# Kernel tuning notes

Hardware: AMD Instinct MI355X
Metric: run time of the kernel (lower is better)

## Reference

```python
import jax, jax.numpy as jnp
import numpy as np

B, T, VOCAB = 65536, 34, 14
D_MODEL, TOK_DIM, POS_DIM, QK_DIM, FFN = 5, 2, 3, 5, 2
MAX_DIGITS = 10
EPS = 1e-5


def setup_inputs() -> dict:
    key = jax.random.key(0)
    ks = jax.random.split(key, 8)
    return dict(
        idx=jax.random.randint(ks[0], (B, T), 0, VOCAB),
        tok_A=jnp.float32(2.5), tok_start=jnp.float32(-1.2), tok_stride=jnp.float32(0.29),
        sp_amp=jnp.float32(3.5), sp_phase=jnp.float32(0.0), sp_slope=jnp.float32(0.15), sp_offset=jnp.float32(0.0),
        norm_w=jnp.ones((D_MODEL,), jnp.float32),
        q_w=jax.random.normal(ks[1], (QK_DIM, POS_DIM), jnp.float32) * 0.5,
        q_phase=jnp.zeros((1,), jnp.float32),
        out_A=jax.random.normal(ks[2], (D_MODEL, 1), jnp.float32) * 0.45,
        out_B=jax.random.normal(ks[3], (1, D_MODEL), jnp.float32) * 0.2,
        fc1_w=jax.random.normal(ks[4], (FFN, D_MODEL), jnp.float32) * 0.4,
        fc2_w=jax.random.normal(ks[5], (D_MODEL, FFN), jnp.float32) * 0.4,
        head_w=jax.random.normal(ks[6], (TOK_DIM, D_MODEL), jnp.float32) * 0.4,
    )


def rmsnorm(x, w):
    rms = jnp.sqrt(jnp.mean(x * x, axis=-1, keepdims=True) + EPS)
    return x / rms * w


def micro_forward(idx, tok_A, tok_start, tok_stride, sp_amp, sp_phase, sp_slope, sp_offset,
                  norm_w, q_w, q_phase, out_A, out_B, fc1_w, fc2_w, head_w):
    # token arc embedding table (V, 2)
    d = jnp.arange(VOCAB, dtype=jnp.float32)
    ang = tok_start + d * tok_stride
    tok_emb = jnp.stack([tok_A * jnp.cos(ang), tok_A * jnp.sin(ang)], axis=-1)
    # spiral positional embedding (T, 3)
    t = jnp.arange(T, dtype=jnp.float32)
    th = 2.0 * jnp.pi * t / MAX_DIGITS + sp_phase
    pos = jnp.stack([sp_amp * jnp.cos(th), sp_amp * jnp.sin(th), sp_slope * t + sp_offset], axis=-1)
    # embed: concat token (B,T,2) + position (T,3) -> (B,T,5)
    x = jnp.concatenate([tok_emb[idx], jnp.broadcast_to(pos, (idx.shape[0], T, POS_DIM))], axis=-1)
    # attention (pre-norm); q/k from positions only (qk_input='pos'), shared across batch
    h = rmsnorm(x, norm_w)
    k = pos @ q_w.T                       # (T, QK)
    c, s = jnp.cos(q_phase[0]), jnp.sin(q_phase[0])
    q = k.at[:, 0].set(c * k[:, 0] - s * k[:, 1]).at[:, 1].set(s * k[:, 0] + c * k[:, 1])
    scores = (q @ k.T) / jnp.sqrt(jnp.float32(QK_DIM))   # (T, T)
    causal = jnp.tril(jnp.ones((T, T), bool))
    attn = jax.nn.softmax(jnp.where(causal, scores, -1e9), axis=-1)
    attn_out = jnp.einsum('ts,bsd->btd', attn, h)         # v = normed x (head_dim = d_model)
    x = x + (attn_out @ out_A) @ out_B                    # rank-1 out_proj, residual
    # FFN (pre-norm, 2 hidden units)
    h2 = rmsnorm(x, norm_w)
    x = x + jax.nn.relu(h2 @ fc1_w.T) @ fc2_w.T
    # head: project to token plane, read out against arc embedding table
    hf = rmsnorm(x, norm_w)
    logits = (hf @ head_w.T) @ tok_emb.T                  # (B, T, V)
    return logits


def reference(idx, tok_A, tok_start, tok_stride, sp_amp, sp_phase, sp_slope, sp_offset,
              norm_w, q_w, q_phase, out_A, out_B, fc1_w, fc2_w, head_w):
    return micro_forward(idx, tok_A, tok_start, tok_stride, sp_amp, sp_phase, sp_slope, sp_offset,
                         norm_w, q_w, q_phase, out_A, out_B, fc1_w, fc2_w, head_w)
```

## Files before the change

### kernel.cpp

```cpp
#include <hip/hip_runtime.h>
#include <math.h>

#define T 34
#define V 14
#define NT 256
#define NBLK 1088
#define NWAVES 4352
#define KTILES 8
#define NPAIRS 4
#define LIM (65536 * 34)

typedef float f32x4 __attribute__((ext_vector_type(4)));

__global__ __launch_bounds__(NT, 4) void micro_fused(
    const int* __restrict__ idx, float* __restrict__ out,
    const float* __restrict__ p_tokA, const float* __restrict__ p_tokStart,
    const float* __restrict__ p_tokStride, const float* __restrict__ p_spAmp,
    const float* __restrict__ p_spPhase, const float* __restrict__ p_spSlope,
    const float* __restrict__ p_spOffset, const float* __restrict__ norm_w,
    const float* __restrict__ q_w, const float* __restrict__ q_phase,
    const float* __restrict__ out_A, const float* __restrict__ out_B,
    const float* __restrict__ fc1_w, const float* __restrict__ fc2_w,
    const float* __restrict__ head_w)
{
    __shared__ float G_lds[V * 35];
    __shared__ float TE_lds[V * 2];
    __shared__ float POS_lds[T * 3];
    __shared__ float gbW[4][2][104];
    __shared__ float stageAll[4 * 896];

    const int tid = threadIdx.x;
    const int w = tid >> 6, lane = tid & 63;
    const int wid = blockIdx.x * 4 + w;

    float* sA = stageAll;
    float* sK = stageAll + 1200;
    float* sQ = stageAll + 1370;

    if (tid < V) {
        float ang = p_tokStart[0] + (float)tid * p_tokStride[0];
        TE_lds[2 * tid]     = p_tokA[0] * cosf(ang);
        TE_lds[2 * tid + 1] = p_tokA[0] * sinf(ang);
    }
    if (tid < T) {
        float th = (float)tid * 0.62831853071795864769f + p_spPhase[0];
        float p0 = p_spAmp[0] * cosf(th), p1 = p_spAmp[0] * sinf(th);
        float p2 = p_spSlope[0] * (float)tid + p_spOffset[0];
        POS_lds[3 * tid] = p0; POS_lds[3 * tid + 1] = p1; POS_lds[3 * tid + 2] = p2;
        float kk[5];
        #pragma unroll
        for (int i = 0; i < 5; ++i)
            kk[i] = p0 * q_w[3 * i] + p1 * q_w[3 * i + 1] + p2 * q_w[3 * i + 2];
        float cc = cosf(q_phase[0]), ss = sinf(q_phase[0]);
        #pragma unroll
        for (int i = 0; i < 5; ++i) sK[tid * 5 + i] = kk[i];
        sQ[tid * 5 + 0] = cc * kk[0] - ss * kk[1];
        sQ[tid * 5 + 1] = ss * kk[0] + cc * kk[1];
        sQ[tid * 5 + 2] = kk[2]; sQ[tid * 5 + 3] = kk[3]; sQ[tid * 5 + 4] = kk[4];
    }
    __syncthreads();

    for (int e = tid; e < T * T; e += NT) {
        unsigned tt = (unsigned)e / (unsigned)T;
        unsigned s  = (unsigned)e - tt * T;
        float d = 0.f;
        #pragma unroll
        for (int i = 0; i < 5; ++i) d += sQ[tt * 5 + i] * sK[s * 5 + i];
        sA[tt * 35 + s] = (s <= tt) ? d * 0.44721359549995793928f : 0.f;
    }
    for (int e = tid; e < V * 35; e += NT) {
        int v = e / 35, s = e - v * 35;
        float g = 0.f;
        if (s < T) {
            float x0 = TE_lds[2*v], x1 = TE_lds[2*v+1];
            float x2 = POS_lds[3*s], x3 = POS_lds[3*s+1], x4 = POS_lds[3*s+2];
            float ms = (x0*x0 + x1*x1 + x2*x2 + x3*x3 + x4*x4) * 0.2f;
            float r = rsqrtf(ms + 1e-5f);
            g = (x0 * norm_w[0] * out_A[0] + x1 * norm_w[1] * out_A[1]
               + x2 * norm_w[2] * out_A[2] + x3 * norm_w[3] * out_A[3]
               + x4 * norm_w[4] * out_A[4]) * r;
        }
        G_lds[e] = g;
    }
    __syncthreads();

    const int t = (wid * 64 + lane) % T;
    float A[T];
    #pragma unroll
    for (int s = 0; s < T; ++s) A[s] = sA[t * 35 + s];
    {
        float mx = -1e30f;
        #pragma unroll
        for (int s = 0; s < T; ++s) if (s <= t) mx = fmaxf(mx, A[s]);
        float sum = 0.f;
        #pragma unroll
        for (int s = 0; s < T; ++s) {
            float e2 = (s <= t) ? expf(A[s] - mx) : 0.f;
            A[s] = e2;
            sum += e2;
        }
        float inv = 1.f / sum;
        #pragma unroll
        for (int s = 0; s < T; ++s) A[s] *= inv;
    }
    const float ps0 = POS_lds[3*t], ps1 = POS_lds[3*t+1], ps2 = POS_lds[3*t+2];
    float te0[V], te1[V];
    #pragma unroll
    for (int v = 0; v < V; ++v) { te0[v] = TE_lds[2*v]; te1[v] = TE_lds[2*v+1]; }
    __syncthreads();

    const float nw0 = norm_w[0], nw1 = norm_w[1], nw2 = norm_w[2], nw3 = norm_w[3], nw4 = norm_w[4];
    const float oB0 = out_B[0], oB1 = out_B[1], oB2 = out_B[2], oB3 = out_B[3], oB4 = out_B[4];
    float w1[2][5], hw[2][5], w20[5], w21[5];
    #pragma unroll
    for (int j = 0; j < 2; ++j)
        #pragma unroll
        for (int d = 0; d < 5; ++d) { w1[j][d] = fc1_w[j*5+d]; hw[j][d] = head_w[j*5+d]; }
    #pragma unroll
    for (int d = 0; d < 5; ++d) { w20[d] = fc2_w[2*d]; w21[d] = fc2_w[2*d+1]; }

    const int s_a = (lane < T) ? lane : lane - T;
    const int i2 = lane + 64;
    const int s_b = (i2 < 68) ? i2 - 34 : i2 - 68;
    const bool act2 = (i2 < 102);

    float* gbA = gbW[w][0];
    float* gbB = gbW[w][1];
    float* stg = stageAll + w * 896;
    float2* stg2 = reinterpret_cast<float2*>(stg);
    const f32x4* st4 = reinterpret_cast<const f32x4*>(stg);

    auto computeItem = [&](int tile, int rbase, int curtok, const float* gbT) {
        float acc0 = 0.f, acc1 = 0.f;
        const float2* gbp = reinterpret_cast<const float2*>(gbT + rbase);
        #pragma unroll
        for (int s = 0; s < 17; ++s) {
            float2 gg = gbp[s];
            acc0 = fmaf(A[2*s],   gg.x, acc0);
            acc1 = fmaf(A[2*s+1], gg.y, acc1);
        }
        float acc = acc0 + acc1;

        float2 te = *reinterpret_cast<const float2*>(&TE_lds[curtok * 2]);
        float x0 = te.x + acc * oB0;
        float x1 = te.y + acc * oB1;
        float x2 = ps0 + acc * oB2;
        float x3 = ps1 + acc * oB3;
        float x4 = ps2 + acc * oB4;

        float ms = (x0*x0 + x1*x1 + x2*x2 + x3*x3 + x4*x4) * 0.2f;
        float rr = rsqrtf(ms + 1e-5f);
        float h0 = x0*rr*nw0, h1 = x1*rr*nw1, h2 = x2*rr*nw2, h3 = x3*rr*nw3, h4 = x4*rr*nw4;
        float f0 = fmaxf(0.f, h0*w1[0][0] + h1*w1[0][1] + h2*w1[0][2] + h3*w1[0][3] + h4*w1[0][4]);
        float f1 = fmaxf(0.f, h0*w1[1][0] + h1*w1[1][1] + h2*w1[1][2] + h3*w1[1][3] + h4*w1[1][4]);
        x0 += f0*w20[0] + f1*w21[0];
        x1 += f0*w20[1] + f1*w21[1];
        x2 += f0*w20[2] + f1*w21[2];
        x3 += f0*w20[3] + f1*w21[3];
        x4 += f0*w20[4] + f1*w21[4];

        ms = (x0*x0 + x1*x1 + x2*x2 + x3*x3 + x4*x4) * 0.2f;
        rr = rsqrtf(ms + 1e-5f);
        h0 = x0*rr*nw0; h1 = x1*rr*nw1; h2 = x2*rr*nw2; h3 = x3*rr*nw3; h4 = x4*rr*nw4;
        float p0 = h0*hw[0][0] + h1*hw[0][1] + h2*hw[0][2] + h3*hw[0][3] + h4*hw[0][4];
        float p1 = h0*hw[1][0] + h1*hw[1][1] + h2*hw[1][2] + h3*hw[1][3] + h4*hw[1][4];

        #pragma unroll
        for (int j = 0; j < 7; ++j) {
            float2 o2;
            o2.x = p0 * te0[2*j]   + p1 * te1[2*j];
            o2.y = p0 * te0[2*j+1] + p1 * te1[2*j+1];
            stg2[lane * 7 + j] = o2;
        }
        f32x4* outp = reinterpret_cast<f32x4*>(out) + (size_t)tile * 224;
        __builtin_nontemporal_store(st4[lane],       outp + lane);
        __builtin_nontemporal_store(st4[lane + 64],  outp + lane + 64);
        __builtin_nontemporal_store(st4[lane + 128], outp + lane + 128);
        if (lane < 32)
            __builtin_nontemporal_store(st4[lane + 192], outp + lane + 192);
    };

    int tileA = wid, tileB = wid + NWAVES;
    int b0A = (tileA * 64) / T, b0B = (tileB * 64) / T;
    int tk0A = idx[b0A * T + lane];
    int tk1A = idx[min(b0A * T + lane + 64, LIM - 1)];
    int tkoA = idx[tileA * 64 + lane];
    int tk0B = idx[b0B * T + lane];
    int tk1B = idx[min(b0B * T + lane + 64, LIM - 1)];
    int tkoB = idx[tileB * 64 + lane];

    #pragma unroll
    for (int it = 0; it < NPAIRS; ++it) {
        gbA[lane] = G_lds[tk0A * 35 + s_a];
        if (act2) gbA[i2] = G_lds[tk1A * 35 + s_b];
        gbB[lane] = G_lds[tk0B * 35 + s_a];
        if (act2) gbB[i2] = G_lds[tk1B * 35 + s_b];

        const int rbA = ((tileA * 64 + lane) / T - b0A) * T;
        const int rbB = ((tileB * 64 + lane) / T - b0B) * T;
        const int ctA = tkoA, ctB = tkoB;
        const int tA = tileA, tB = tileB;

        if (it < NPAIRS - 1) {
            tileA += 2 * NWAVES; tileB += 2 * NWAVES;
            b0A = (tileA * 64) / T; b0B = (tileB * 64) / T;
            tk0A = idx[b0A * T + lane];
            tk1A = idx[min(b0A * T + lane + 64, LIM - 1)];
            tkoA = idx[tileA * 64 + lane];
            tk0B = idx[b0B * T + lane];
            tk1B = idx[min(b0B * T + lane + 64, LIM - 1)];
            tkoB = idx[tileB * 64 + lane];
        }

        computeItem(tA, rbA, ctA, gbA);
        computeItem(tB, rbB, ctB, gbB);
    }
}

extern "C" void kernel_launch(void* const* d_in, const int* in_sizes, int n_in,
                              void* d_out, int out_size, void* d_ws, size_t ws_size,
                              hipStream_t stream) {
    const int*   idx        = (const int*)  d_in[0];
    const float* tok_A      = (const float*)d_in[1];
    const float* tok_start  = (const float*)d_in[2];
    const float* tok_stride = (const float*)d_in[3];
    const float* sp_amp     = (const float*)d_in[4];
    const float* sp_phase   = (const float*)d_in[5];
    const float* sp_slope   = (const float*)d_in[6];
    const float* sp_offset  = (const float*)d_in[7];
    const float* norm_w     = (const float*)d_in[8];
    const float* q_w        = (const float*)d_in[9];
    const float* q_phase    = (const float*)d_in[10];
    const float* out_A      = (const float*)d_in[11];
    const float* out_B      = (const float*)d_in[12];
    const float* fc1_w      = (const float*)d_in[13];
    const float* fc2_w      = (const float*)d_in[14];
    const float* head_w     = (const float*)d_in[15];
    float* out = (float*)d_out;

    micro_fused<<<NBLK, NT, 0, stream>>>(idx, out, tok_A, tok_start, tok_stride,
                                         sp_amp, sp_phase, sp_slope, sp_offset,
                                         norm_w, q_w, q_phase, out_A, out_B,
                                         fc1_w, fc2_w, head_w);
}
```

Before: 35.94 us.

## Store logits directly from registers and double-buffer G staging with deeper idx prefetch

Drops the per-wave LDS staging buffer and the coalesced nontemporal float4 stores. Each lane now writes its 7 float2 logits straight to global memory, and the LDS footprint shrinks because the scratch area is reused for the gather buffers. The G gather buffers are double-buffered, and idx loads are prefetched two pairs ahead, so the next pair's staging overlaps the current pair's dot products. In exchange, stores are strided per lane (56-byte stride) rather than fully contiguous, and they lose the nontemporal hint.

```diff
diff --git a/kernel.cpp b/kernel.cpp
--- a/kernel.cpp
+++ b/kernel.cpp
@@ -6,11 +6,8 @@
 #define NT 256
 #define NBLK 1088
 #define NWAVES 4352
-#define KTILES 8
 #define NPAIRS 4
 #define LIM (65536 * 34)
-
-typedef float f32x4 __attribute__((ext_vector_type(4)));
 
 __global__ __launch_bounds__(NT, 4) void micro_fused(
     const int* __restrict__ idx, float* __restrict__ out,
@@ -26,16 +23,15 @@
     __shared__ float G_lds[V * 35];
     __shared__ float TE_lds[V * 2];
     __shared__ float POS_lds[T * 3];
-    __shared__ float gbW[4][2][104];
-    __shared__ float stageAll[4 * 896];
+    __shared__ float scratch[1700];
 
     const int tid = threadIdx.x;
     const int w = tid >> 6, lane = tid & 63;
     const int wid = blockIdx.x * 4 + w;
 
-    float* sA = stageAll;
-    float* sK = stageAll + 1200;
-    float* sQ = stageAll + 1370;
+    float* sA = scratch;
+    float* sK = scratch + 1200;
+    float* sQ = scratch + 1370;
 
     if (tid < V) {
         float ang = p_tokStart[0] + (float)tid * p_tokStride[0];
@@ -124,13 +120,22 @@
     const int s_b = (i2 < 68) ? i2 - 34 : i2 - 68;
     const bool act2 = (i2 < 102);
 
-    float* gbA = gbW[w][0];
-    float* gbB = gbW[w][1];
-    float* stg = stageAll + w * 896;
-    float2* stg2 = reinterpret_cast<float2*>(stg);
-    const f32x4* st4 = reinterpret_cast<const f32x4*>(stg);
-
-    auto computeItem = [&](int tile, int rbase, int curtok, const float* gbT) {
+    float* gbBase = scratch + w * 416;
+
+    auto tkLoad = [&](int p, int ab, int& t0, int& t1, int& to) {
+        int tile = wid + (2 * p + ab) * NWAVES;
+        int b0 = (tile * 64) / T;
+        t0 = idx[b0 * T + lane];
+        t1 = idx[min(b0 * T + lane + 64, LIM - 1)];
+        to = idx[tile * 64 + lane];
+    };
+    auto stagePair = [&](int t0A, int t1A, int t0B, int t1B, float* gA, float* gB) {
+        gA[lane] = G_lds[t0A * 35 + s_a];
+        if (act2) gA[i2] = G_lds[t1A * 35 + s_b];
+        gB[lane] = G_lds[t0B * 35 + s_a];
+        if (act2) gB[i2] = G_lds[t1B * 35 + s_b];
+    };
+    auto dot = [&](const float* gbT, int rbase) -> float {
         float acc0 = 0.f, acc1 = 0.f;
         const float2* gbp = reinterpret_cast<const float2*>(gbT + rbase);
         #pragma unroll
@@ -139,8 +144,9 @@
             acc0 = fmaf(A[2*s],   gg.x, acc0);
             acc1 = fmaf(A[2*s+1], gg.y, acc1);
         }
-        float acc = acc0 + acc1;
-
+        return acc0 + acc1;
+    };
+    auto epiStore = [&](int tile, int curtok, float acc) {
         float2 te = *reinterpret_cast<const float2*>(&TE_lds[curtok * 2]);
         float x0 = te.x + acc * oB0;
         float x1 = te.y + acc * oB1;
@@ -165,55 +171,50 @@
         float p0 = h0*hw[0][0] + h1*hw[0][1] + h2*hw[0][2] + h3*hw[0][3] + h4*hw[0][4];
         float p1 = h0*hw[1][0] + h1*hw[1][1] + h2*hw[1][2] + h3*hw[1][3] + h4*hw[1][4];
 
+        float2* op = reinterpret_cast<float2*>(out) + (size_t)tile * 448 + lane * 7;
         #pragma unroll
         for (int j = 0; j < 7; ++j) {
             float2 o2;
             o2.x = p0 * te0[2*j]   + p1 * te1[2*j];
             o2.y = p0 * te0[2*j+1] + p1 * te1[2*j+1];
-            stg2[lane * 7 + j] = o2;
-        }
-        f32x4* outp = reinterpret_cast<f32x4*>(out) + (size_t)tile * 224;
-        __builtin_nontemporal_store(st4[lane],       outp + lane);
-        __builtin_nontemporal_store(st4[lane + 64],  outp + lane + 64);
-        __builtin_nontemporal_store(st4[lane + 128], outp + lane + 128);
-        if (lane < 32)
-            __builtin_nontemporal_store(st4[lane + 192], outp + lane + 192);
-    };
-
-    int tileA = wid, tileB = wid + NWAVES;
-    int b0A = (tileA * 64) / T, b0B = (tileB * 64) / T;
-    int tk0A = idx[b0A * T + lane];
-    int tk1A = idx[min(b0A * T + lane + 64, LIM - 1)];
-    int tkoA = idx[tileA * 64 + lane];
-    int tk0B = idx[b0B * T + lane];
-    int tk1B = idx[min(b0B * T + lane + 64, LIM - 1)];
-    int tkoB = idx[tileB * 64 + lane];
+            op[j] = o2;
+        }
+    };
+
+    int c_t0A, c_t1A, c_toA, c_t0B, c_t1B, c_toB;
+    int n_t0A, n_t1A, n_toA, n_t0B, n_t1B, n_toB;
+    tkLoad(0, 0, c_t0A, c_t1A, c_toA);
+    tkLoad(0, 1, c_t0B, c_t1B, c_toB);
+    stagePair(c_t0A, c_t1A, c_t0B, c_t1B, gbBase, gbBase + 104);
+    tkLoad(1, 0, n_t0A, n_t1A, n_toA);
+    tkLoad(1, 1, n_t0B, n_t1B, n_toB);
 
     #pragma unroll
     for (int it = 0; it < NPAIRS; ++it) {
-        gbA[lane] = G_lds[tk0A * 35 + s_a];
-        if (act2) gbA[i2] = G_lds[tk1A * 35 + s_b];
-        gbB[lane] = G_lds[tk0B * 35 + s_a];
-        if (act2) gbB[i2] = G_lds[tk1B * 35 + s_b];
-
+        float* gA = gbBase + (it & 1) * 208;
+        float* gB = gA + 104;
+        const int tileA = wid + (2 * it)     * NWAVES;
+        const int tileB = wid + (2 * it + 1) * NWAVES;
+        const int b0A = (tileA * 64) / T, b0B = (tileB * 64) / T;
         const int rbA = ((tileA * 64 + lane) / T - b0A) * T;
         const int rbB = ((tileB * 64 + lane) / T - b0B) * T;
-        const int ctA = tkoA, ctB = tkoB;
-        const int tA = tileA, tB = tileB;
+        const int ctA = c_toA, ctB = c_toB;
+
+        float accA = dot(gA, rbA);
+        float accB = dot(gB, rbB);
 
         if (it < NPAIRS - 1) {
-            tileA += 2 * NWAVES; tileB += 2 * NWAVES;
-            b0A = (tileA * 64) / T; b0B = (tileB * 64) / T;
-            tk0A = idx[b0A * T + lane];
-            tk1A = idx[min(b0A * T + lane + 64, LIM - 1)];
-            tkoA = idx[tileA * 64 + lane];
-            tk0B = idx[b0B * T + lane];
-            tk1B = idx[min(b0B * T + lane + 64, LIM - 1)];
-            tkoB = idx[tileB * 64 + lane];
-        }
-
-        computeItem(tA, rbA, ctA, gbA);
-        computeItem(tB, rbB, ctB, gbB);
+            float* ngA = gbBase + ((it + 1) & 1) * 208;
+            stagePair(n_t0A, n_t1A, n_t0B, n_t1B, ngA, ngA + 104);
+            c_toA = n_toA; c_toB = n_toB;
+            if (it < NPAIRS - 2) {
+                tkLoad(it + 2, 0, n_t0A, n_t1A, n_toA);
+                tkLoad(it + 2, 1, n_t0B, n_t1B, n_toB);
+            }
+        }
+
+        epiStore(tileA, ctA, accA);
+        epiStore(tileB, ctB, accB);
     }
 }
 
```

Result: slower. 73.77 us (+105.2%).

## Double-buffer gather and output staging to overlap index loads, compute and stores

Applied to the files above, without the earlier changes.

Restructures the per-wave loop into a software pipeline. Token indices are prefetched two iterations ahead, the G gather is staged into a double buffer one iteration ahead, and the output staging is split into two buffers so the copy-out of one tile is interleaved with the epilogue of the next. The goal is to hide global load latency and LDS round trips behind arithmetic. The cost is doubled LDS use per block (about 20 KB of staging), which may lower occupancy, plus more live registers for the prefetched indices.

```diff
diff --git a/kernel.cpp b/kernel.cpp
--- a/kernel.cpp
+++ b/kernel.cpp
@@ -6,7 +6,6 @@
 #define NT 256
 #define NBLK 1088
 #define NWAVES 4352
-#define KTILES 8
 #define NPAIRS 4
 #define LIM (65536 * 34)
 
@@ -26,16 +25,16 @@
     __shared__ float G_lds[V * 35];
     __shared__ float TE_lds[V * 2];
     __shared__ float POS_lds[T * 3];
-    __shared__ float gbW[4][2][104];
-    __shared__ float stageAll[4 * 896];
+    __shared__ float gbW[4][2][208];
+    __shared__ float stageW[4][2][896];
 
     const int tid = threadIdx.x;
     const int w = tid >> 6, lane = tid & 63;
     const int wid = blockIdx.x * 4 + w;
 
-    float* sA = stageAll;
-    float* sK = stageAll + 1200;
-    float* sQ = stageAll + 1370;
+    float* sA = &stageW[0][0][0];
+    float* sK = sA + 1200;
+    float* sQ = sA + 1370;
 
     if (tid < V) {
         float ang = p_tokStart[0] + (float)tid * p_tokStride[0];
@@ -124,13 +123,24 @@
     const int s_b = (i2 < 68) ? i2 - 34 : i2 - 68;
     const bool act2 = (i2 < 102);
 
-    float* gbA = gbW[w][0];
-    float* gbB = gbW[w][1];
-    float* stg = stageAll + w * 896;
-    float2* stg2 = reinterpret_cast<float2*>(stg);
-    const f32x4* st4 = reinterpret_cast<const f32x4*>(stg);
-
-    auto computeItem = [&](int tile, int rbase, int curtok, const float* gbT) {
+    auto loadTok = [&](int p, int& t0A, int& t1A, int& toA, int& t0B, int& t1B, int& toB) {
+        int tA = wid + (2 * p)     * NWAVES;
+        int tB = wid + (2 * p + 1) * NWAVES;
+        int bA = (tA * 64) / T, bB = (tB * 64) / T;
+        t0A = idx[bA * T + lane];
+        t1A = idx[min(bA * T + lane + 64, LIM - 1)];
+        toA = idx[tA * 64 + lane];
+        t0B = idx[bB * T + lane];
+        t1B = idx[min(bB * T + lane + 64, LIM - 1)];
+        toB = idx[tB * 64 + lane];
+    };
+    auto stageP = [&](float* dst, int t0A, int t1A, int t0B, int t1B) {
+        dst[lane] = G_lds[t0A * 35 + s_a];
+        if (act2) dst[i2] = G_lds[t1A * 35 + s_b];
+        dst[104 + lane] = G_lds[t0B * 35 + s_a];
+        if (act2) dst[104 + i2] = G_lds[t1B * 35 + s_b];
+    };
+    auto dot = [&](const float* gbT, int rbase) -> float {
         float acc0 = 0.f, acc1 = 0.f;
         const float2* gbp = reinterpret_cast<const float2*>(gbT + rbase);
         #pragma unroll
@@ -139,8 +149,9 @@
             acc0 = fmaf(A[2*s],   gg.x, acc0);
             acc1 = fmaf(A[2*s+1], gg.y, acc1);
         }
-        float acc = acc0 + acc1;
-
+        return acc0 + acc1;
+    };
+    auto epi = [&](float* stg, int curtok, float acc) {
         float2 te = *reinterpret_cast<const float2*>(&TE_lds[curtok * 2]);
         float x0 = te.x + acc * oB0;
         float x1 = te.y + acc * oB1;
@@ -165,6 +176,7 @@
         float p0 = h0*hw[0][0] + h1*hw[0][1] + h2*hw[0][2] + h3*hw[0][3] + h4*hw[0][4];
         float p1 = h0*hw[1][0] + h1*hw[1][1] + h2*hw[1][2] + h3*hw[1][3] + h4*hw[1][4];
 
+        float2* stg2 = reinterpret_cast<float2*>(stg);
         #pragma unroll
         for (int j = 0; j < 7; ++j) {
             float2 o2;
@@ -172,6 +184,9 @@
             o2.y = p0 * te0[2*j+1] + p1 * te1[2*j+1];
             stg2[lane * 7 + j] = o2;
         }
+    };
+    auto copyout = [&](int tile, const float* stg) {
+        const f32x4* st4 = reinterpret_cast<const f32x4*>(stg);
         f32x4* outp = reinterpret_cast<f32x4*>(out) + (size_t)tile * 224;
         __builtin_nontemporal_store(st4[lane],       outp + lane);
         __builtin_nontemporal_store(st4[lane + 64],  outp + lane + 64);
@@ -180,41 +195,38 @@
             __builtin_nontemporal_store(st4[lane + 192], outp + lane + 192);
     };
 
-    int tileA = wid, tileB = wid + NWAVES;
-    int b0A = (tileA * 64) / T, b0B = (tileB * 64) / T;
-    int tk0A = idx[b0A * T + lane];
-    int tk1A = idx[min(b0A * T + lane + 64, LIM - 1)];
-    int tkoA = idx[tileA * 64 + lane];
-    int tk0B = idx[b0B * T + lane];
-    int tk1B = idx[min(b0B * T + lane + 64, LIM - 1)];
-    int tkoB = idx[tileB * 64 + lane];
+    int c_t0A, c_t1A, c_toA, c_t0B, c_t1B, c_toB;
+    int n_t0A, n_t1A, n_toA, n_t0B, n_t1B, n_toB;
+    loadTok(0, c_t0A, c_t1A, c_toA, c_t0B, c_t1B, c_toB);
+    stageP(gbW[w][0], c_t0A, c_t1A, c_t0B, c_t1B);
+    loadTok(1, n_t0A, n_t1A, n_toA, n_t0B, n_t1B, n_toB);
+    int curToA = c_toA, curToB = c_toB;
 
     #pragma unroll
     for (int it = 0; it < NPAIRS; ++it) {
-        gbA[lane] = G_lds[tk0A * 35 + s_a];
-        if (act2) gbA[i2] = G_lds[tk1A * 35 + s_b];
-        gbB[lane] = G_lds[tk0B * 35 + s_a];
-        if (act2) gbB[i2] = G_lds[tk1B * 35 + s_b];
-
-        const int rbA = ((tileA * 64 + lane) / T - b0A) * T;
-        const int rbB = ((tileB * 64 + lane) / T - b0B) * T;
-        const int ctA = tkoA, ctB = tkoB;
-        const int tA = tileA, tB = tileB;
+        float* g = gbW[w][it & 1];
+        const int tX = wid + (2 * it)     * NWAVES;
+        const int tY = wid + (2 * it + 1) * NWAVES;
+        const int rbX = ((tX * 64 + lane) / T - (tX * 64) / T) * T;
+        const int rbY = ((tY * 64 + lane) / T - (tY * 64) / T) * T;
+
+        float accX = dot(g,       rbX);
+        float accY = dot(g + 104, rbY);
+        const int ctX = curToA, ctY = curToB;
 
         if (it < NPAIRS - 1) {
-            tileA += 2 * NWAVES; tileB += 2 * NWAVES;
-            b0A = (tileA * 64) / T; b0B = (tileB * 64) / T;
-            tk0A = idx[b0A * T + lane];
-            tk1A = idx[min(b0A * T + lane + 64, LIM - 1)];
-            tkoA = idx[tileA * 64 + lane];
-            tk0B = idx[b0B * T + lane];
-            tk1B = idx[min(b0B * T + lane + 64, LIM - 1)];
-            tkoB = idx[tileB * 64 + lane];
-        }
-
-        computeItem(tA, rbA, ctA, gbA);
-        computeItem(tB, rbB, ctB, gbB);
-    }
+            stageP(gbW[w][(it + 1) & 1], n_t0A, n_t1A, n_t0B, n_t1B);
+            curToA = n_toA; curToB = n_toB;
+            if (it < NPAIRS - 2)
+                loadTok(it + 2, n_t0A, n_t1A, n_toA, n_t0B, n_t1B, n_toB);
+        }
+
+        epi(stageW[w][0], ctX, accX);
+        if (it > 0) copyout(tY - 2 * NWAVES, stageW[w][1]);
+        epi(stageW[w][1], ctY, accY);
+        copyout(tX, stageW[w][0]);
+    }
+    copyout(wid + 7 * NWAVES, stageW[w][1]);
 }
 
 extern "C" void kernel_launch(void* const* d_in, const int* in_sizes, int n_in,
```

Result: slower. 74.61 us (+107.6%).
